# Kernel optimization log

Measured on AMD Instinct MI355X. Metric: run time of the kernel, lower is better.

Reference implementation:

```python
import jax, jax.numpy as jnp
import numpy as np

NUM_HEADS = 16
ROPE_THETA = 10000.0


def _rope_cos_sin(seq_len, head_dim, dtype):
    # Llama rotary embedding: inv_freq over even dims, emb = cat(freqs, freqs)
    inv_freq = 1.0 / (ROPE_THETA ** (jnp.arange(0, head_dim, 2, dtype=jnp.float32) / head_dim))
    t = jnp.arange(seq_len, dtype=jnp.float32)
    freqs = jnp.outer(t, inv_freq)              # [S, hd/2]
    emb = jnp.concatenate([freqs, freqs], -1)   # [S, hd]
    return jnp.cos(emb).astype(dtype), jnp.sin(emb).astype(dtype)


def _rotate_half(x):
    h = x.shape[-1] // 2
    return jnp.concatenate([-x[..., h:], x[..., :h]], axis=-1)


def setup_inputs() -> dict:
    key = jax.random.key(0)
    ks = jax.random.split(key, 5)
    B, S, D = 1, 2048, 2048
    scale = 0.02
    return {
        "hidden_states": jax.random.normal(ks[0], (B, S, D), jnp.float32),
        "Wq": jax.random.normal(ks[1], (D, D), jnp.float32) * scale,
        "Wk": jax.random.normal(ks[2], (D, D), jnp.float32) * scale,
        "Wv": jax.random.normal(ks[3], (D, D), jnp.float32) * scale,
        "Wo": jax.random.normal(ks[4], (D, D), jnp.float32) * scale,
    }


def reference(hidden_states, Wq, Wk, Wv, Wo):
    B, S, D = hidden_states.shape
    H = NUM_HEADS
    hd = D // H
    sm_scale = 1.0 / np.sqrt(hd)

    # QKV projections (nn.Linear without bias: x @ W.T), kept in [B,S,H,hd]
    q = (hidden_states @ Wq.T).reshape(B, S, H, hd)
    k = (hidden_states @ Wk.T).reshape(B, S, H, hd)
    v = (hidden_states @ Wv.T).reshape(B, S, H, hd)

    # RoPE (offset=0, no kv cache)
    cos, sin = _rope_cos_sin(S, hd, hidden_states.dtype)
    cos = cos[None, :, None, :]  # [1,S,1,hd]
    sin = sin[None, :, None, :]
    q = q * cos + _rotate_half(q) * sin
    k = k * cos + _rotate_half(k) * sin

    # Causal self-attention (exact math of FlashSelfAttention(causal=True))
    scores = jnp.einsum("bshd,bthd->bhst", q, k) * sm_scale  # [B,H,S,S]
    causal = jnp.tril(jnp.ones((S, S), dtype=bool))
    scores = jnp.where(causal[None, None], scores, jnp.finfo(scores.dtype).min)
    probs = jax.nn.softmax(scores, axis=-1)
    attn = jnp.einsum("bhst,bthd->bshd", probs, v)           # [B,S,H,hd]

    # Output projection
    attn = attn.reshape(B, S, H * hd)
    return attn @ Wo.T
```

## Files before the change

### kernel.cpp

```cpp
#include <hip/hip_runtime.h>
#include <hip/hip_bf16.h>
#include <math.h>

#define S_LEN 2048
#define DMODEL 2048
#define NHEADS 16
#define HDIM 128

typedef __bf16 bf16x8 __attribute__((ext_vector_type(8)));
typedef float f32x4 __attribute__((ext_vector_type(4)));
typedef float f32x16 __attribute__((ext_vector_type(16)));

__device__ __forceinline__ unsigned short f2b(float f) {
  union { float f; unsigned u; } c; c.f = f;
  unsigned r = (c.u + 0x7fffu + ((c.u >> 16) & 1u)) >> 16;
  return (unsigned short)r;
}
__device__ __forceinline__ float b2f(unsigned short b) {
  union { unsigned u; float f; } c; c.u = ((unsigned)b) << 16;
  return c.f;
}

__device__ __forceinline__ void gload_lds16(const unsigned short* g, unsigned short* l) {
  __builtin_amdgcn_global_load_lds(
      (__attribute__((address_space(1))) void*)(void*)g,
      (__attribute__((address_space(3))) void*)(void*)l, 16, 0, 0);
}

__global__ void cvt5_f32_bf16_k(const float* __restrict__ s0,
                                const float* __restrict__ s1,
                                const float* __restrict__ s2,
                                const float* __restrict__ s3,
                                const float* __restrict__ s4,
                                unsigned short* __restrict__ d0,
                                unsigned short* __restrict__ d1,
                                unsigned short* __restrict__ d2,
                                unsigned short* __restrict__ d3,
                                unsigned short* __restrict__ d4) {
  int gi = blockIdx.x * blockDim.x + threadIdx.x;
  int seg = gi >> 20;
  int i = (gi & 0xFFFFF) * 4;
  const float* src = (seg == 0) ? s0 : (seg == 1) ? s1 : (seg == 2) ? s2
                     : (seg == 3) ? s3 : s4;
  unsigned short* dst = (seg == 0) ? d0 : (seg == 1) ? d1 : (seg == 2) ? d2
                        : (seg == 3) ? d3 : d4;
  float4 v = *reinterpret_cast<const float4*>(src + i);
  ushort4 o;
  o.x = f2b(v.x); o.y = f2b(v.y); o.z = f2b(v.z); o.w = f2b(v.w);
  *reinterpret_cast<ushort4*>(dst + i) = o;
}

__global__ void addf2_k(const float* __restrict__ a, const float* __restrict__ b,
                        float* __restrict__ out) {
  int i = (blockIdx.x * blockDim.x + threadIdx.x) * 4;
  float4 x = *reinterpret_cast<const float4*>(a + i);
  float4 y = *reinterpret_cast<const float4*>(b + i);
  x.x += y.x; x.y += y.y; x.z += y.z; x.w += y.w;
  *reinterpret_cast<float4*>(out + i) = x;
}

__global__ void rope_table_k(float* __restrict__ cs, float* __restrict__ sn) {
  int idx = blockIdx.x * blockDim.x + threadIdx.x;
  int s = idx >> 6, i = idx & 63;
  float inv = powf(10000.0f, -(float)(2 * i) / 128.0f);
  float a = (float)s * inv;
  cs[idx] = cosf(a);
  sn[idx] = sinf(a);
}

__global__ void rope_apply_k(unsigned short* __restrict__ q,
                             unsigned short* __restrict__ k,
                             const float* __restrict__ cs,
                             const float* __restrict__ sn) {
  const float SC = 0.08838834764831845f * 1.4426950408889634f;
  int idx = blockIdx.x * blockDim.x + threadIdx.x;
  int i = idx & 63;
  int h = (idx >> 6) & (NHEADS - 1);
  int s = idx >> 10;
  size_t base = (size_t)s * DMODEL + h * HDIM;
  float c = cs[s * 64 + i], sv = sn[s * 64 + i];
  float qc = c * SC, qs = sv * SC;
  float q1 = b2f(q[base + i]), q2 = b2f(q[base + i + 64]);
  q[base + i]      = f2b(q1 * qc - q2 * qs);
  q[base + i + 64] = f2b(q2 * qc + q1 * qs);
  float k1 = b2f(k[base + i]), k2 = b2f(k[base + i + 64]);
  k[base + i]      = f2b(k1 * c - k2 * sv);
  k[base + i + 64] = f2b(k2 * c + k1 * sv);
}

__global__ __launch_bounds__(256) void transpose_bf16_k(
    const unsigned short* __restrict__ in, unsigned short* __restrict__ out) {
  __shared__ unsigned short tile[64][72];
  int bx = blockIdx.x, by = blockIdx.y;
  int t = threadIdx.x;
#pragma unroll
  for (int i = 0; i < 2; ++i) {
    int ch = i * 256 + t;
    int r = ch >> 3, c8 = ch & 7;
    bf16x8 v = *reinterpret_cast<const bf16x8*>(
        in + (size_t)(by * 64 + r) * DMODEL + bx * 64 + c8 * 8);
    *reinterpret_cast<bf16x8*>(&tile[r][c8 * 8]) = v;
  }
  __syncthreads();
#pragma unroll
  for (int i = 0; i < 2; ++i) {
    int ch = i * 256 + t;
    int c = ch >> 3, r8 = ch & 7;
    union { bf16x8 v; unsigned short u[8]; } w;
#pragma unroll
    for (int j = 0; j < 8; ++j) w.u[j] = tile[r8 * 8 + j][c];
    *reinterpret_cast<bf16x8*>(
        out + (size_t)(bx * 64 + c) * S_LEN + by * 64 + r8 * 8) = w.v;
  }
}


#define MIDBAR_SEQ()                                      \
  do {                                                    \
    asm volatile("" ::: "memory");                        \
    __builtin_amdgcn_s_barrier();                         \
    asm volatile("s_waitcnt lgkmcnt(0)" ::: "memory");    \
    __builtin_amdgcn_s_setprio(1);                        \
  } while (0)

#define ENDBAR_SEQ()                                      \
  do {                                                    \
    __builtin_amdgcn_s_setprio(0);                        \
    asm volatile("" ::: "memory");                        \
    __builtin_amdgcn_s_barrier();                         \
    asm volatile("" ::: "memory");                        \
  } while (0)

#define READA(QM)                                                              \
  do {                                                                         \
    _Pragma("unroll") for (int j = 0; j < MQ; ++j)                             \
    _Pragma("unroll") for (int kk = 0; kk < 2; ++kk) {                         \
      int row = wm * (BM / 2) + ((QM) * MQ + j) * 16 + li;                     \
      int c = (kk * 4 + g) ^ (li & 7);                                         \
      af[j][kk] = *reinterpret_cast<const bf16x8*>(&As[cur][row * 64 + c * 8]);\
    }                                                                          \
  } while (0)

#define READB(BF, QN)                                                          \
  do {                                                                         \
    _Pragma("unroll") for (int jn = 0; jn < 2; ++jn)                           \
    _Pragma("unroll") for (int kk = 0; kk < 2; ++kk) {                         \
      int row = wn * 64 + ((QN) * 2 + jn) * 16 + li;                           \
      int c = (kk * 4 + g) ^ (li & 7);                                         \
      BF[jn][kk] = *reinterpret_cast<const bf16x8*>(&Bs[cur][row * 64 + c * 8]);\
    }                                                                          \
  } while (0)

#define QUAD(QM, QN, BF)                                                       \
  do {                                                                         \
    _Pragma("unroll") for (int j = 0; j < MQ; ++j)                             \
    _Pragma("unroll") for (int jn = 0; jn < 2; ++jn)                           \
    _Pragma("unroll") for (int kk = 0; kk < 2; ++kk)                           \
      acc[(QM) * MQ + j][(QN) * 2 + jn] =                                      \
          __builtin_amdgcn_mfma_f32_16x16x32_bf16(                             \
              af[j][kk], BF[jn][kk], acc[(QM) * MQ + j][(QN) * 2 + jn], 0, 0, 0);\
  } while (0)

template <int BM, bool OUT_F32>
__global__ __launch_bounds__(512, 2) void gemm_8ph_k(
    const unsigned short* __restrict__ A, const unsigned short* __restrict__ B0p,
    const unsigned short* __restrict__ B1p, const unsigned short* __restrict__ B2p,
    void* __restrict__ C0, void* __restrict__ C1, void* __restrict__ C2,
    int M, int N, int Kl, int Kstr, int aoffz) {
  constexpr int MQ = BM / 64;
  constexpr int MR = BM / 32;

  __shared__ unsigned short As[2][BM * 64];
  __shared__ unsigned short Bs[2][256 * 64];

  const unsigned short* Ap = A + (size_t)blockIdx.z * aoffz;
  const unsigned short* Bp = (blockIdx.z == 0) ? B0p : (blockIdx.z == 1) ? B1p : B2p;
  void* Cout = (blockIdx.z == 0) ? C0 : (blockIdx.z == 1) ? C1 : C2;

  int bid = blockIdx.x;
  int tm = bid >> 3;
  int tn = ((bid & 7) + 3 * (int)blockIdx.z) & 7;
  int m0 = tm * BM, n0 = tn << 8;

  const int tid = threadIdx.x;
  const int wave = tid >> 6, lane = tid & 63;
  const int g = lane >> 4, li = lane & 15;
  const int wm = wave >> 2, wn = wave & 3;

  auto stageB = [&](int buf, int tt, int qn) {
#pragma unroll
    for (int i = 0; i < 2; ++i) {
      int j = i * 512 + tid;
      int piece = j >> 8, rowin = (j >> 3) & 31, c = j & 7;
      int row = piece * 64 + qn * 32 + rowin;
      gload_lds16(Bp + (size_t)(n0 + row) * Kstr + tt * 64 + ((c ^ (row & 7)) * 8),
                  &Bs[buf][row * 64 + c * 8]);
    }
  };
  auto stageA = [&](int buf, int tt, int qm) {
#pragma unroll
    for (int i = 0; i < BM / 128; ++i) {
      int j = i * 512 + tid;
      int piece = j / (2 * BM);
      int rowin = (j >> 3) & (BM / 4 - 1);
      int c = j & 7;
      int row = piece * (BM / 2) + qm * (BM / 4) + rowin;
      gload_lds16(Ap + (size_t)(m0 + row) * Kstr + tt * 64 + ((c ^ (row & 7)) * 8),
                  &As[buf][row * 64 + c * 8]);
    }
  };

  f32x4 acc[MR][4];
#pragma unroll
  for (int i = 0; i < MR; ++i)
#pragma unroll
    for (int j = 0; j < 4; ++j) acc[i][j] = (f32x4){0.f, 0.f, 0.f, 0.f};

  const int nK = Kl >> 6;

  stageB(0, 0, 0); stageA(0, 0, 0); stageB(0, 0, 1); stageA(0, 0, 1);
  stageB(1, 1, 0); stageA(1, 1, 0); stageB(1, 1, 1); stageA(1, 1, 1);
  if constexpr (BM == 256) asm volatile("s_waitcnt vmcnt(8)" ::: "memory");
  else                     asm volatile("s_waitcnt vmcnt(6)" ::: "memory");
  asm volatile("" ::: "memory");
  __builtin_amdgcn_s_barrier();
  asm volatile("" ::: "memory");

  for (int t = 0; t < nK; ++t) {
    int cur = t & 1;
    bool pf = (t + 2 < nK);
    bf16x8 af[MQ][2], bf0[2][2], bf1[2][2];
    READA(0);
    READB(bf0, 0);
    MIDBAR_SEQ();
    QUAD(0, 0, bf0);
    ENDBAR_SEQ();
    READB(bf1, 1);
    if (pf) { stageB(cur, t + 2, 0); stageA(cur, t + 2, 0); }
    MIDBAR_SEQ();
    QUAD(0, 1, bf1);
    ENDBAR_SEQ();
    READA(1);
    if (pf) stageB(cur, t + 2, 1);
    MIDBAR_SEQ();
    QUAD(1, 1, bf1);
    ENDBAR_SEQ();
    if (pf) {
      stageA(cur, t + 2, 1);
      if constexpr (BM == 256) asm volatile("s_waitcnt vmcnt(8)" ::: "memory");
      else                     asm volatile("s_waitcnt vmcnt(6)" ::: "memory");
    } else {
      asm volatile("s_waitcnt vmcnt(0)" ::: "memory");
    }
    MIDBAR_SEQ();
    QUAD(1, 0, bf0);
    ENDBAR_SEQ();
  }

#pragma unroll
  for (int m = 0; m < MR; ++m) {
#pragma unroll
    for (int n = 0; n < 4; ++n) {
      int row = m0 + wm * (BM / 2) + m * 16 + g * 4;
      int col = n0 + wn * 64 + n * 16 + li;
#pragma unroll
      for (int r = 0; r < 4; ++r) {
        if (OUT_F32)
          reinterpret_cast<float*>(Cout)[(size_t)(row + r) * N + col] = acc[m][n][r];
        else
          reinterpret_cast<unsigned short*>(Cout)[(size_t)(row + r) * N + col] =
              f2b(acc[m][n][r]);
      }
    }
  }
}

#undef MIDBAR_SEQ
#undef ENDBAR_SEQ
#undef READA
#undef READB
#undef QUAD

__global__ __launch_bounds__(256) void flash_attn_k(
    const unsigned short* __restrict__ q, const unsigned short* __restrict__ k,
    const unsigned short* __restrict__ vt, unsigned short* __restrict__ o) {
  __shared__ unsigned short Ks[2][2][32 * 128];
  __shared__ unsigned short Vs[2][2][128 * 32];

  int L = blockIdx.x;
  int xcd = L & 7, j = L >> 3;
  int h = 2 * xcd + (j & 1);
  int qt = (j < 32) ? (31 - (j >> 1)) : ((j - 32) >> 1);

  int t = threadIdx.x, wave = t >> 6, l = t & 63;
  int l5 = l >> 5, l31 = l & 31;
  int par = wave >> 1, qh = wave & 1;
  int q0 = qt * 64;
  int q_abs = q0 + qh * 32 + l31;

  const unsigned short* vth = vt + (size_t)h * HDIM * S_LEN;

  auto stage = [&](int buf, int it) {
#pragma unroll
    for (int p2 = 0; p2 < 2; ++p2) {
      int kv0 = it * 64 + p2 * 32;
#pragma unroll
      for (int i = 0; i < 2; ++i) {
        int ch = i * 256 + t;
        int row = ch >> 4, c = ch & 15;
        gload_lds16(k + (size_t)(kv0 + row) * DMODEL + h * HDIM + ((c ^ (row & 7)) * 8),
                    &Ks[p2][buf][ch * 8]);
      }
#pragma unroll
      for (int i = 0; i < 2; ++i) {
        int ch = i * 256 + t;
        int row = ch >> 2, c = ch & 3;
        gload_lds16(vth + (size_t)row * S_LEN + kv0 + ((c ^ (row & 3)) * 8),
                    &Vs[p2][buf][ch * 8]);
      }
    }
  };

  bf16x8 qf[8];
#pragma unroll
  for (int kb = 0; kb < 8; ++kb)
    qf[kb] = *reinterpret_cast<const bf16x8*>(
        q + (size_t)q_abs * DMODEL + h * HDIM + kb * 16 + l5 * 8);

  f32x16 OT[4];
#pragma unroll
  for (int nf = 0; nf < 4; ++nf)
#pragma unroll
    for (int r = 0; r < 16; ++r) OT[nf][r] = 0.f;
  float m_r = -1e30f, l_r = 0.f;

  int nIter = qt + 1;
  stage(0, 0);

  for (int it = 0; it < nIter; ++it) {
    int cur = it & 1;
    if (it + 1 < nIter) {
      stage(cur ^ 1, it + 1);
      asm volatile("s_waitcnt vmcnt(8)" ::: "memory");
    } else {
      asm volatile("s_waitcnt vmcnt(0)" ::: "memory");
    }
    __builtin_amdgcn_s_barrier();
    asm volatile("" ::: "memory");

    int kv0 = it * 64 + par * 32;
    f32x16 sf;
#pragma unroll
    for (int r = 0; r < 16; ++r) sf[r] = 0.f;
#pragma unroll
    for (int kb = 0; kb < 8; ++kb) {
      int c = (2 * kb + l5) ^ (l31 & 7);
      bf16x8 kf = *reinterpret_cast<const bf16x8*>(&Ks[par][cur][(l31 * 16 + c) * 8]);
      sf = __builtin_amdgcn_mfma_f32_32x32x16_bf16(kf, qf[kb], sf, 0, 0, 0);
    }
    if (it == qt) {
#pragma unroll
      for (int r = 0; r < 16; ++r) {
        int kv_abs = kv0 + (r & 3) + 8 * (r >> 2) + 4 * l5;
        if (kv_abs > q_abs) sf[r] = -1e30f;
      }
    }
    float pm = -1e30f;
#pragma unroll
    for (int r = 0; r < 16; ++r) pm = fmaxf(pm, sf[r]);
    pm = fmaxf(pm, __shfl_xor(pm, 32));
    if (!__all(pm - m_r <= 8.0f)) {
      float nm = fmaxf(m_r, pm);
      float alpha = exp2f(m_r - nm);
      m_r = nm;
      l_r *= alpha;
#pragma unroll
      for (int nf = 0; nf < 4; ++nf)
#pragma unroll
        for (int r = 0; r < 16; ++r) OT[nf][r] *= alpha;
    }
    float ls = 0.f;
#pragma unroll
    for (int r = 0; r < 16; ++r) {
      float pv = exp2f(sf[r] - m_r);
      sf[r] = pv;
      ls += pv;
    }
    l_r += ls + __shfl_xor(ls, 32);

    bf16x8 pf[2];
#pragma unroll
    for (int ks = 0; ks < 2; ++ks) {
      const int m0 = 8 * ks;
      unsigned A0, A1, B0, B1;
      asm("v_cvt_pk_bf16_f32 %0, %1, %2" : "=v"(A0) : "v"(sf[m0 + 0]), "v"(sf[m0 + 1]));
      asm("v_cvt_pk_bf16_f32 %0, %1, %2" : "=v"(A1) : "v"(sf[m0 + 2]), "v"(sf[m0 + 3]));
      asm("v_cvt_pk_bf16_f32 %0, %1, %2" : "=v"(B0) : "v"(sf[m0 + 4]), "v"(sf[m0 + 5]));
      asm("v_cvt_pk_bf16_f32 %0, %1, %2" : "=v"(B1) : "v"(sf[m0 + 6]), "v"(sf[m0 + 7]));
      unsigned rA0 = (unsigned)__shfl_xor((int)A0, 32);
      unsigned rA1 = (unsigned)__shfl_xor((int)A1, 32);
      unsigned rB0 = (unsigned)__shfl_xor((int)B0, 32);
      unsigned rB1 = (unsigned)__shfl_xor((int)B1, 32);
      union { unsigned u[4]; bf16x8 v; } pk;
      pk.u[0] = l5 ? rB0 : A0;
      pk.u[1] = l5 ? rB1 : A1;
      pk.u[2] = l5 ? B0 : rA0;
      pk.u[3] = l5 ? B1 : rA1;
      pf[ks] = pk.v;
    }

#pragma unroll
    for (int ks = 0; ks < 2; ++ks) {
#pragma unroll
      for (int nf = 0; nf < 4; ++nf) {
        int row = nf * 32 + l31;
        int c = (2 * ks + l5) ^ (row & 3);
        bf16x8 vf = *reinterpret_cast<const bf16x8*>(&Vs[par][cur][(row * 4 + c) * 8]);
        OT[nf] = __builtin_amdgcn_mfma_f32_32x32x16_bf16(vf, pf[ks], OT[nf], 0, 0, 0);
      }
    }
    __builtin_amdgcn_s_barrier();
    asm volatile("" ::: "memory");
  }

  float* MS = (float*)&Ks[0][0][0];
  float* ML = MS + 8192;
  if (par == 1) {
#pragma unroll
    for (int nf = 0; nf < 4; ++nf)
#pragma unroll
      for (int r = 0; r < 16; ++r) {
        int d = nf * 32 + (r & 3) + 8 * (r >> 2) + 4 * l5;
        MS[qh * 4096 + d * 32 + l31] = OT[nf][r];
      }
    if (l < 32) { ML[qh * 64 + l31] = m_r; ML[qh * 64 + 32 + l31] = l_r; }
  }
  __builtin_amdgcn_s_barrier();
  asm volatile("" ::: "memory");
  if (par == 0) {
    float mB = ML[qh * 64 + l31], lB = ML[qh * 64 + 32 + l31];
    float ms = fmaxf(m_r, mB);
    float eA = exp2f(m_r - ms), eB = exp2f(mB - ms);
    float inv = 1.0f / (l_r * eA + lB * eB);
#pragma unroll
    for (int nf = 0; nf < 4; ++nf)
#pragma unroll
      for (int r = 0; r < 16; ++r) {
        int d = nf * 32 + (r & 3) + 8 * (r >> 2) + 4 * l5;
        OT[nf][r] = (OT[nf][r] * eA + MS[qh * 4096 + d * 32 + l31] * eB) * inv;
      }
  }
  __builtin_amdgcn_s_barrier();
  asm volatile("" ::: "memory");
  if (par == 0) {
#pragma unroll
    for (int nf = 0; nf < 4; ++nf)
#pragma unroll
      for (int r = 0; r < 16; ++r) {
        int d = nf * 32 + (r & 3) + 8 * (r >> 2) + 4 * l5;
        MS[qh * 4096 + d * 32 + l31] = OT[nf][r];
      }
  }
  __builtin_amdgcn_s_barrier();
  asm volatile("" ::: "memory");
  {
    int qq = t >> 2;
    int dg = (t & 3) * 32;
    const float* src = MS + (qq >> 5) * 4096 + (qq & 31);
    unsigned pk[16];
#pragma unroll
    for (int i = 0; i < 16; ++i) {
      unsigned lo = f2b(src[(dg + 2 * i) * 32]);
      unsigned hi = f2b(src[(dg + 2 * i + 1) * 32]);
      pk[i] = lo | (hi << 16);
    }
    unsigned short* op = o + (size_t)(q0 + qq) * DMODEL + h * HDIM + dg;
#pragma unroll
    for (int i = 0; i < 4; ++i) {
      uint4 w = make_uint4(pk[4 * i], pk[4 * i + 1], pk[4 * i + 2], pk[4 * i + 3]);
      *reinterpret_cast<uint4*>(op + i * 8) = w;
    }
  }
}

extern "C" void kernel_launch(void* const* d_in, const int* in_sizes, int n_in,
                              void* d_out, int out_size, void* d_ws, size_t ws_size,
                              hipStream_t stream) {
  const float* hs = (const float*)d_in[0];
  const float* Wq = (const float*)d_in[1];
  const float* Wk = (const float*)d_in[2];
  const float* Wv = (const float*)d_in[3];
  const float* Wo = (const float*)d_in[4];

  char* ws = (char*)d_ws;
  const size_t MB = 1024 * 1024;
  unsigned short* hs_b = (unsigned short*)(ws + 0 * MB);
  unsigned short* Wq_b = (unsigned short*)(ws + 8 * MB);
  unsigned short* Wk_b = (unsigned short*)(ws + 16 * MB);
  unsigned short* Wv_b = (unsigned short*)(ws + 24 * MB);
  unsigned short* Wo_b = (unsigned short*)(ws + 32 * MB);
  unsigned short* qb = (unsigned short*)(ws + 40 * MB);
  unsigned short* kb = (unsigned short*)(ws + 48 * MB);
  unsigned short* vb = (unsigned short*)(ws + 56 * MB);
  unsigned short* ab = (unsigned short*)(ws + 64 * MB);
  float* cs = (float*)(ws + 72 * MB);
  float* sn = (float*)(ws + 72 * MB + 512 * 1024);
  unsigned short* vtb = hs_b;
  float* P0 = (float*)(ws + 8 * MB);
  float* P1 = (float*)(ws + 40 * MB);

  cvt5_f32_bf16_k<<<(5 * 1024 * 1024) / 256, 256, 0, stream>>>(
      hs, Wq, Wk, Wv, Wo, hs_b, Wq_b, Wk_b, Wv_b, Wo_b);

  rope_table_k<<<(S_LEN * 64) / 256, 256, 0, stream>>>(cs, sn);

  gemm_8ph_k<256, false><<<dim3(64, 1, 3), 512, 0, stream>>>(
      hs_b, Wq_b, Wk_b, Wv_b, qb, kb, vb, 2048, 2048, 2048, 2048, 0);

  transpose_bf16_k<<<dim3(32, 32), 256, 0, stream>>>(vb, vtb);

  rope_apply_k<<<(S_LEN * NHEADS * 64) / 256, 256, 0, stream>>>(qb, kb, cs, sn);

  flash_attn_k<<<dim3(512), 256, 0, stream>>>(qb, kb, vtb, ab);

  gemm_8ph_k<128, true><<<dim3(128, 1, 2), 512, 0, stream>>>(
      ab, Wo_b, Wo_b + 1024, Wo_b, P0, P1, P0, 2048, 2048, 1024, 2048, 1024);
  addf2_k<<<(2048 * 2048) / 1024, 256, 0, stream>>>(P0, P1, (float*)d_out);
}
```

Before: 198.3 us.

## Load K and V fragments directly from global memory instead of LDS staging

Removes the double-buffered LDS staging of K and V tiles (async global-to-LDS copies, waitcnt and block barriers) from the flash attention loop. Each wave now reads its K and V MFMA operands straight from global memory, leaving LDS only for the final cross-wave merge buffer. This cuts LDS use and barrier synchronisation, which may raise occupancy, but loses the prefetch overlap and exposes global load latency directly before each MFMA.

```diff
diff --git a/kernel.cpp b/kernel.cpp
--- a/kernel.cpp
+++ b/kernel.cpp
@@ -284,8 +284,7 @@
 __global__ __launch_bounds__(256) void flash_attn_k(
     const unsigned short* __restrict__ q, const unsigned short* __restrict__ k,
     const unsigned short* __restrict__ vt, unsigned short* __restrict__ o) {
-  __shared__ unsigned short Ks[2][2][32 * 128];
-  __shared__ unsigned short Vs[2][2][128 * 32];
+  __shared__ float MS[2 * 4096 + 128];
 
   int L = blockIdx.x;
   int xcd = L & 7, j = L >> 3;
@@ -299,27 +298,7 @@
   int q_abs = q0 + qh * 32 + l31;
 
   const unsigned short* vth = vt + (size_t)h * HDIM * S_LEN;
-
-  auto stage = [&](int buf, int it) {
-#pragma unroll
-    for (int p2 = 0; p2 < 2; ++p2) {
-      int kv0 = it * 64 + p2 * 32;
-#pragma unroll
-      for (int i = 0; i < 2; ++i) {
-        int ch = i * 256 + t;
-        int row = ch >> 4, c = ch & 15;
-        gload_lds16(k + (size_t)(kv0 + row) * DMODEL + h * HDIM + ((c ^ (row & 7)) * 8),
-                    &Ks[p2][buf][ch * 8]);
-      }
-#pragma unroll
-      for (int i = 0; i < 2; ++i) {
-        int ch = i * 256 + t;
-        int row = ch >> 2, c = ch & 3;
-        gload_lds16(vth + (size_t)row * S_LEN + kv0 + ((c ^ (row & 3)) * 8),
-                    &Vs[p2][buf][ch * 8]);
-      }
-    }
-  };
+  const unsigned short* krow = k + (size_t)l31 * DMODEL + h * HDIM + l5 * 8;
 
   bf16x8 qf[8];
 #pragma unroll
@@ -335,27 +314,17 @@
   float m_r = -1e30f, l_r = 0.f;
 
   int nIter = qt + 1;
-  stage(0, 0);
 
   for (int it = 0; it < nIter; ++it) {
-    int cur = it & 1;
-    if (it + 1 < nIter) {
-      stage(cur ^ 1, it + 1);
-      asm volatile("s_waitcnt vmcnt(8)" ::: "memory");
-    } else {
-      asm volatile("s_waitcnt vmcnt(0)" ::: "memory");
-    }
-    __builtin_amdgcn_s_barrier();
-    asm volatile("" ::: "memory");
-
     int kv0 = it * 64 + par * 32;
+
     f32x16 sf;
 #pragma unroll
     for (int r = 0; r < 16; ++r) sf[r] = 0.f;
 #pragma unroll
     for (int kb = 0; kb < 8; ++kb) {
-      int c = (2 * kb + l5) ^ (l31 & 7);
-      bf16x8 kf = *reinterpret_cast<const bf16x8*>(&Ks[par][cur][(l31 * 16 + c) * 8]);
+      bf16x8 kf = *reinterpret_cast<const bf16x8*>(
+          krow + (size_t)kv0 * DMODEL + kb * 16);
       sf = __builtin_amdgcn_mfma_f32_32x32x16_bf16(kf, qf[kb], sf, 0, 0, 0);
     }
     if (it == qt) {
@@ -413,17 +382,13 @@
     for (int ks = 0; ks < 2; ++ks) {
 #pragma unroll
       for (int nf = 0; nf < 4; ++nf) {
-        int row = nf * 32 + l31;
-        int c = (2 * ks + l5) ^ (row & 3);
-        bf16x8 vf = *reinterpret_cast<const bf16x8*>(&Vs[par][cur][(row * 4 + c) * 8]);
+        bf16x8 vf = *reinterpret_cast<const bf16x8*>(
+            vth + (size_t)(nf * 32 + l31) * S_LEN + kv0 + (2 * ks + l5) * 8);
         OT[nf] = __builtin_amdgcn_mfma_f32_32x32x16_bf16(vf, pf[ks], OT[nf], 0, 0, 0);
       }
     }
-    __builtin_amdgcn_s_barrier();
-    asm volatile("" ::: "memory");
-  }
-
-  float* MS = (float*)&Ks[0][0][0];
+  }
+
   float* ML = MS + 8192;
   if (par == 1) {
 #pragma unroll
```

Result: slower. 219.3 us (+10.6%).
